# Kernel tuning notes

Measured on AMD Instinct MI355X. Metric: run time of the kernel, lower is better.

Reference implementation:

```python
import math
import jax, jax.numpy as jnp
import numpy as np

S, D = 4096, 2048
H, DH = 16, 128
ROPE_BASE = 10000.0


def _rotate_half(x):
    # x: [..., dh]; pairs (x1, x2) -> (-x2, x1), interleaved
    shp = x.shape
    x = x.reshape(*shp[:-1], shp[-1] // 2, 2)
    x1, x2 = x[..., 0], x[..., 1]
    return jnp.stack((-x2, x1), axis=-1).reshape(shp)


def _rope_cos_sin(seq_len, dh):
    inv_freq = 1.0 / (ROPE_BASE ** (jnp.arange(0, dh, 2, dtype=jnp.float32) / dh))
    t = jnp.arange(seq_len, dtype=jnp.float32)
    freqs = jnp.einsum('i,j->ij', t, inv_freq)  # [S, dh/2]
    cos = jnp.repeat(jnp.cos(freqs), 2, axis=-1)  # [S, dh]
    sin = jnp.repeat(jnp.sin(freqs), 2, axis=-1)
    return cos, sin


def setup_inputs() -> dict:
    key = jax.random.key(0)
    kx, kq, kk, kv, ko = jax.random.split(key, 5)
    scale_in = 1.0 / math.sqrt(D)
    scale_hd = 1.0 / math.sqrt(H * DH)
    return {
        'x': jax.random.normal(kx, (S, D), dtype=jnp.float32),
        'mask': jnp.tril(jnp.ones((S, S), dtype=bool)),  # causal
        'wq': jax.random.normal(kq, (H * DH, D), dtype=jnp.float32) * scale_in,
        'wk': jax.random.normal(kk, (H * DH, D), dtype=jnp.float32) * scale_in,
        'wv': jax.random.normal(kv, (H * DH, D), dtype=jnp.float32) * scale_in,
        'wo': jax.random.normal(ko, (D, H * DH), dtype=jnp.float32) * scale_hd,
    }


def reference(x, mask, wq, wk, wv, wo):
    s = x.shape[0]
    # QKV projections (Linear: y = W @ x per token) -> [h, S, dh]
    q = (x @ wq.T).reshape(s, H, DH).transpose(1, 0, 2)
    k = (x @ wk.T).reshape(s, H, DH).transpose(1, 0, 2)
    v = (x @ wv.T).reshape(s, H, DH).transpose(1, 0, 2)
    # RoPE
    cos, sin = _rope_cos_sin(s, DH)  # [S, dh] each
    q = q * cos[None] + _rotate_half(q) * sin[None]
    k = k * cos[None] + _rotate_half(k) * sin[None]
    # Attention
    sim = jnp.einsum('hid,hjd->hij', q, k) / math.sqrt(DH)  # [h, S, S]
    sim = jnp.where(mask[None], sim, -jnp.inf)
    attn = jax.nn.softmax(sim, axis=-1)
    out = jnp.einsum('hij,hjd->ihd', attn, v).reshape(s, H * DH)
    return out @ wo.T
```

## Files before the change

### kernel.cpp

```cpp
#include <hip/hip_runtime.h>
#include <stdint.h>

#define S_LEN 4096
#define D_MODEL 2048
#define NH 16
#define DH 128

typedef short s16x8 __attribute__((ext_vector_type(8)));
typedef short s16x2 __attribute__((ext_vector_type(2)));
typedef unsigned short u16;
typedef unsigned short u16x4 __attribute__((ext_vector_type(4)));
typedef float f32x4 __attribute__((ext_vector_type(4)));

__device__ __forceinline__ u16 f2bf(float f) {
  union { float f; uint32_t u; } v; v.f = f;
  uint32_t u = v.u;
  u += 0x7FFFu + ((u >> 16) & 1u);
  return (u16)(u >> 16);
}

__device__ __forceinline__ float bf2f(u16 b) {
  union { uint32_t u; float f; } v; v.u = ((uint32_t)b) << 16;
  return v.f;
}

__device__ __forceinline__ void async_copy16(const u16* g, u16* l) {
  __builtin_amdgcn_global_load_lds(
      (const __attribute__((address_space(1))) unsigned int*)g,
      (__attribute__((address_space(3))) unsigned int*)l, 16, 0, 0);
}

__global__ void cast_kernel(const float4* __restrict__ src, u16* __restrict__ dst, int n4) {
  int i = blockIdx.x * blockDim.x + threadIdx.x;
  if (i >= n4) return;
  float4 v = src[i];
  u16x4 o;
  o[0] = f2bf(v.x); o[1] = f2bf(v.y); o[2] = f2bf(v.z); o[3] = f2bf(v.w);
  *(u16x4*)(dst + (size_t)i * 4) = o;
}

__global__ void cast4_kernel(const float4* __restrict__ s0, const float4* __restrict__ s1,
                             const float4* __restrict__ s2, const float4* __restrict__ s3,
                             u16* __restrict__ d0, u16* __restrict__ d1,
                             u16* __restrict__ d2, u16* __restrict__ d3) {
  int b = blockIdx.x;
  int which = b >> 12;
  const float4* src = which == 0 ? s0 : which == 1 ? s1 : which == 2 ? s2 : s3;
  u16* dst = which == 0 ? d0 : which == 1 ? d1 : which == 2 ? d2 : d3;
  int i = (b & 4095) * blockDim.x + threadIdx.x;
  float4 v = src[i];
  u16x4 o;
  o[0] = f2bf(v.x); o[1] = f2bf(v.y); o[2] = f2bf(v.z); o[3] = f2bf(v.w);
  *(u16x4*)(dst + (size_t)i * 4) = o;
}

__global__ void rope_table(float* __restrict__ ctab, float* __restrict__ stab) {
  int idx = blockIdx.x * blockDim.x + threadIdx.x;
  int t = idx >> 6, p = idx & 63;
  float invf = powf(10000.0f, -(float)p / 64.0f);
  float th = (float)t * invf;
  ctab[idx] = cosf(th);
  stab[idx] = sinf(th);
}

#define PH_LGK0() do { asm volatile("s_waitcnt lgkmcnt(0)" ::: "memory"); \
                       __builtin_amdgcn_sched_barrier(0); } while (0)

__device__ __forceinline__ void stage16k(const u16* __restrict__ src, u16* dstbase,
                                         const int K) {
  const int tid = threadIdx.x;
  int rr = tid >> 3;
  int gc = ((tid & 7) ^ (rr & 7)) << 3;
  const u16* s = src + (size_t)rr * K + gc;
  u16* d = dstbase + (tid << 3);
  async_copy16(s, d);
  async_copy16(s + (size_t)64 * K, d + 4096);
}

__device__ __forceinline__ void mma256x128(
    const u16* __restrict__ Ab, const u16* __restrict__ Bb,
    const int K, u16* lds, f32x4 (&acc)[4][4])
{
  const int tid = threadIdx.x;
  const int lane = tid & 63, quad = lane >> 4, l16 = lane & 15;
  const int w = tid >> 6, wr = w >> 1, wc = w & 1;

  u16* const A0 = lds;
  u16* const B0 = lds + 16384;
  u16* const A1 = lds + 24576;
  u16* const B1 = lds + 40960;
  const int NT = K >> 6;

  auto sA = [&](int t, u16* buf) {
    int tc = t < NT ? t : NT - 1;
    stage16k(Ab + ((size_t)tc << 6), buf, K);
    stage16k(Ab + (size_t)128 * K + ((size_t)tc << 6), buf + 8192, K);
  };
  auto sB = [&](int t, u16* buf) {
    int tc = t < NT ? t : NT - 1;
    stage16k(Bb + ((size_t)tc << 6), buf, K);
  };

  s16x8 aC[4][2], aN[4][2], bA[2][2], bB0[2][2], bB1[2][2];

  auto rdA = [&](const u16* buf, s16x8 (&a)[4][2]) {
#pragma unroll
    for (int mt = 0; mt < 4; ++mt) {
      int ra = (wr << 6) + (mt << 4) + l16;
#pragma unroll
      for (int ks = 0; ks < 2; ++ks)
        a[mt][ks] = *(const s16x8*)(buf + (ra << 6) + ((((ks << 2) + quad) ^ (ra & 7)) << 3));
    }
  };
  auto rdBh = [&](const u16* buf, int nh, s16x8 (&b)[2][2]) {
#pragma unroll
    for (int nt = 0; nt < 2; ++nt) {
      int rb = (wc << 6) + (((nh << 1) + nt) << 4) + l16;
#pragma unroll
      for (int ks = 0; ks < 2; ++ks)
        b[nt][ks] = *(const s16x8*)(buf + (rb << 6) + ((((ks << 2) + quad) ^ (rb & 7)) << 3));
    }
  };
  auto mmah = [&](s16x8 (&a)[4][2], s16x8 (&b)[2][2], int nh) {
#pragma unroll
    for (int mt = 0; mt < 4; ++mt)
#pragma unroll
      for (int nt = 0; nt < 2; ++nt)
#pragma unroll
        for (int ks = 0; ks < 2; ++ks)
          acc[mt][(nh << 1) + nt] = __builtin_amdgcn_mfma_f32_16x16x32_bf16(
              a[mt][ks], b[nt][ks], acc[mt][(nh << 1) + nt], 0, 0, 0);
  };

  sA(0, A0); sB(0, B0); sA(1, A1); sB(1, B1);
  asm volatile("s_waitcnt vmcnt(6)" ::: "memory");
  __builtin_amdgcn_s_barrier();
  rdA(A0, aC); rdBh(B0, 0, bA); rdBh(B0, 1, bB0);

  const int NI = K >> 7;
#pragma unroll 1
  for (int i = 0; i < NI; ++i) {
    const int t0 = 2 * i, t1 = 2 * i + 1;
    __builtin_amdgcn_s_barrier();
    PH_LGK0();
    __builtin_amdgcn_s_setprio(1);
    mmah(aC, bA, 0);
    __builtin_amdgcn_s_setprio(0);
    asm volatile("s_waitcnt vmcnt(0)" ::: "memory");
    __builtin_amdgcn_s_barrier();
    __builtin_amdgcn_s_barrier();
    PH_LGK0();
    __builtin_amdgcn_s_setprio(1);
    sA(t0 + 2, A0); sB(t0 + 2, B0);
    rdA(A1, aN); rdBh(B1, 0, bA); rdBh(B1, 1, bB1);
    mmah(aC, bB0, 1);
    __builtin_amdgcn_s_setprio(0);
    __builtin_amdgcn_s_barrier();
    __builtin_amdgcn_s_barrier();
    PH_LGK0();
    __builtin_amdgcn_s_setprio(1);
    mmah(aN, bA, 0);
    __builtin_amdgcn_s_setprio(0);
    asm volatile("s_waitcnt vmcnt(0)" ::: "memory");
    __builtin_amdgcn_s_barrier();
    __builtin_amdgcn_s_barrier();
    PH_LGK0();
    __builtin_amdgcn_s_setprio(1);
    sA(t1 + 2, A1); sB(t1 + 2, B1);
    if (i + 1 < NI) { rdA(A0, aC); rdBh(B0, 0, bA); rdBh(B0, 1, bB0); }
    mmah(aN, bB1, 1);
    __builtin_amdgcn_s_setprio(0);
    __builtin_amdgcn_s_barrier();
  }
}

__global__ __launch_bounds__(512) void gemm256_qkv(
    const u16* __restrict__ A,
    const u16* __restrict__ wqb, const u16* __restrict__ wkb, const u16* __restrict__ wvb,
    u16* __restrict__ qh, u16* __restrict__ kh, u16* __restrict__ vh,
    const float* __restrict__ ctab, const float* __restrict__ stab)
{
  __shared__ __align__(16) u16 lds[49152];
  const int tid = threadIdx.x;
  const int lane = tid & 63, quad = lane >> 4, l16 = lane & 15;
  const int w = tid >> 6, wr = w >> 1, wc = w & 1;
  const int m0 = blockIdx.x << 8;
  const int by = blockIdx.y;
  const int which = by >> 4;
  const int n0 = (by & 15) << 7;
  const u16* B = which == 0 ? wqb : which == 1 ? wkb : wvb;
  u16* outp = which == 0 ? qh : which == 1 ? kh : vh;

  f32x4 acc[4][4];
  f32x4 zero = {0.f, 0.f, 0.f, 0.f};
#pragma unroll
  for (int i = 0; i < 4; ++i)
#pragma unroll
    for (int j = 0; j < 4; ++j) acc[i][j] = zero;

  mma256x128(A + (size_t)m0 * D_MODEL, B + (size_t)n0 * D_MODEL, D_MODEL, lds, acc);

#pragma unroll
  for (int mt = 0; mt < 4; ++mt) {
    int rowg = m0 + (wr << 6) + (mt << 4) + (quad << 2);
#pragma unroll
    for (int nt = 0; nt < 4; ++nt) {
      int cl = n0 + (wc << 6) + (nt << 4) + l16;
      int hh = cl >> 7, dd = cl & 127;
      int p = dd >> 1;
      f32x4 v = acc[mt][nt];
#pragma unroll
      for (int r = 0; r < 4; ++r) {
        float val = v[r];
        if (which < 2) {
          float partner = __shfl_xor(val, 1);
          float c = ctab[(size_t)(rowg + r) * 64 + p];
          float s = stab[(size_t)(rowg + r) * 64 + p];
          val = (dd & 1) ? fmaf(val, c, partner * s) : fmaf(val, c, -partner * s);
        }
        outp[((size_t)hh * S_LEN + (rowg + r)) * DH + dd] = f2bf(val);
      }
    }
  }
}

__global__ __launch_bounds__(512) void gemm256_out(
    const u16* __restrict__ A, const u16* __restrict__ B, float* __restrict__ outF)
{
  __shared__ __align__(16) u16 lds[49152];
  const int tid = threadIdx.x;
  const int lane = tid & 63, quad = lane >> 4, l16 = lane & 15;
  const int w = tid >> 6, wr = w >> 1, wc = w & 1;
  const int m0 = blockIdx.x << 8, n0 = blockIdx.y << 7;

  f32x4 acc[4][4];
  f32x4 zero = {0.f, 0.f, 0.f, 0.f};
#pragma unroll
  for (int i = 0; i < 4; ++i)
#pragma unroll
    for (int j = 0; j < 4; ++j) acc[i][j] = zero;

  mma256x128(A + (size_t)m0 * D_MODEL, B + (size_t)n0 * D_MODEL, D_MODEL, lds, acc);

#pragma unroll
  for (int mt = 0; mt < 4; ++mt) {
    int rowg = m0 + (wr << 6) + (mt << 4) + (quad << 2);
#pragma unroll
    for (int nt = 0; nt < 4; ++nt) {
      int col = n0 + (wc << 6) + (nt << 4) + l16;
      f32x4 v = acc[mt][nt];
#pragma unroll
      for (int r = 0; r < 4; ++r) outF[(size_t)(rowg + r) * D_MODEL + col] = v[r];
    }
  }
}

__global__ __launch_bounds__(512) void attn_kernel(
    const u16* __restrict__ Q, const u16* __restrict__ Kb,
    const u16* __restrict__ V,
    u16* __restrict__ U0, u16* __restrict__ U1, float* __restrict__ lbuf)
{
  __shared__ __align__(16) u16 lk[2][64 * 128];
  __shared__ __align__(16) u16 lvt[2][128 * 64];
  __shared__ __align__(16) u16 lp[8 * 1024];

  const int tid = threadIdx.x;
  const int w = tid >> 6, lane = tid & 63, quad = lane >> 4, l16 = lane & 15;
  const int h = blockIdx.y;
  const int bx = blockIdx.x;

  const u16* Qh = Q + (size_t)h * S_LEN * DH;
  const u16* Kh = Kb + (size_t)h * S_LEN * DH;
  const u16* Vh = V + (size_t)h * S_LEN * DH;

  const float scale = 0.08838834764831845f;
  const s16x8 vones = {0x3F80, 0x3F80, 0x3F80, 0x3F80, 0x3F80, 0x3F80, 0x3F80, 0x3F80};
  f32x4 zero = {0.f, 0.f, 0.f, 0.f};
  u16* lpw = lp + (w << 10);

  for (int seg = 0; seg < 2; ++seg) {
    const int qt = seg ? bx : (31 - bx);
    const int jlo = seg ? (qt + 1) : 0;
    const int jhi = seg ? (2 * qt + 2) : (qt + 1);
    const int i0 = qt << 7;
    const int iw = i0 + (w << 4);

    s16x8 qf[4];
#pragma unroll
    for (int ks = 0; ks < 4; ++ks)
      qf[ks] = *(const s16x8*)(Qh + (size_t)(iw + l16) * DH + ks * 32 + quad * 8);

    f32x4 accO[8];
#pragma unroll
    for (int dt = 0; dt < 8; ++dt) accO[dt] = zero;
    f32x4 accL = zero;

    {
      const int j0 = jlo << 6;
      int u = tid & 31, c8 = tid >> 5, r0 = u << 1;
      s16x8 v0 = *(const s16x8*)(Vh + (size_t)(j0 + r0) * DH + (c8 << 3));
      s16x8 v1 = *(const s16x8*)(Vh + (size_t)(j0 + r0 + 1) * DH + (c8 << 3));
#pragma unroll
      for (int rnd = 0; rnd < 2; ++rnd) {
        int c = rnd * 512 + tid;
        int r = c >> 4, cc = c & 15;
        int gcol = ((cc ^ (r & 15)) << 3);
        async_copy16(Kh + (size_t)(j0 + r) * DH + gcol, lk[0] + ((rnd * 512 + w * 64) << 3));
      }
      int cc = r0 >> 3;
#pragma unroll
      for (int e = 0; e < 8; ++e) {
        int d = (c8 << 3) + e;
        int off = (d << 6) + ((cc ^ (d & 7)) << 3) + (r0 & 7);
        s16x2 pr = {v0[e], v1[e]};
        *(s16x2*)(lvt[0] + off) = pr;
      }
    }
    __syncthreads();

    int cur = 0;
    for (int jt = jlo; jt < jhi; ++jt) {
      const int j0 = jt << 6;
      const bool has_next = (jt + 1) < jhi;

      s16x8 nv0, nv1;
      if (has_next) {
        const int nj0 = (jt + 1) << 6;
        int u = tid & 31, c8 = tid >> 5, r0 = u << 1;
        nv0 = *(const s16x8*)(Vh + (size_t)(nj0 + r0) * DH + (c8 << 3));
        nv1 = *(const s16x8*)(Vh + (size_t)(nj0 + r0 + 1) * DH + (c8 << 3));
#pragma unroll
        for (int rnd = 0; rnd < 2; ++rnd) {
          int c = rnd * 512 + tid;
          int r = c >> 4, cc = c & 15;
          int gcol = ((cc ^ (r & 15)) << 3);
          async_copy16(Kh + (size_t)(nj0 + r) * DH + gcol,
                       lk[cur ^ 1] + ((rnd * 512 + w * 64) << 3));
        }
      }

      const u16* lkc = lk[cur];
      f32x4 sa[4];
#pragma unroll
      for (int nt = 0; nt < 4; ++nt) sa[nt] = zero;
      __builtin_amdgcn_s_setprio(1);
#pragma unroll
      for (int ks = 0; ks < 4; ++ks) {
#pragma unroll
        for (int nt = 0; nt < 4; ++nt) {
          int row = (nt << 4) + l16;
          s16x8 kf = *(const s16x8*)(lkc + (row << 7) + ((((ks << 2) + quad) ^ (row & 15)) << 3));
          sa[nt] = __builtin_amdgcn_mfma_f32_16x16x32_bf16(qf[ks], kf, sa[nt], 0, 0, 0);
        }
      }
      __builtin_amdgcn_s_setprio(0);

      const bool maskt = (j0 + 63 > iw);
#pragma unroll
      for (int nt = 0; nt < 4; ++nt) {
        int col = (nt << 4) + l16;
        int j = j0 + col;
        int ccp = col >> 3;
#pragma unroll
        for (int r = 0; r < 4; ++r) {
          float raw = sa[nt][r];
          if (maskt) {
            int i = iw + (quad << 2) + r;
            if (j > i) raw = -1.0e30f;
          }
          float p = __expf(fmaf(raw, scale, -8.0f));
          union { float f; uint32_t u; } pv; pv.f = p;
          int m = (quad << 2) + r;
          lpw[(m << 6) + ((ccp ^ (m & 7)) << 3) + (col & 7)] = (u16)(pv.u >> 16);
        }
      }
      asm volatile("s_waitcnt lgkmcnt(0)" ::: "memory");
      s16x8 pf[2];
#pragma unroll
      for (int kp = 0; kp < 2; ++kp)
        pf[kp] = *(const s16x8*)(lpw + (l16 << 6) + ((((kp << 2) + quad) ^ (l16 & 7)) << 3));

      if (has_next) {
        int u = tid & 31, c8 = tid >> 5, r0 = u << 1;
        int cc = r0 >> 3;
        u16* dst = lvt[cur ^ 1];
#pragma unroll
        for (int e = 0; e < 8; ++e) {
          int d = (c8 << 3) + e;
          int off = (d << 6) + ((cc ^ (d & 7)) << 3) + (r0 & 7);
          s16x2 pr = {nv0[e], nv1[e]};
          *(s16x2*)(dst + off) = pr;
        }
      }

      const u16* lvc = lvt[cur];
      __builtin_amdgcn_s_setprio(1);
      accL = __builtin_amdgcn_mfma_f32_16x16x32_bf16(pf[0], vones, accL, 0, 0, 0);
      accL = __builtin_amdgcn_mfma_f32_16x16x32_bf16(pf[1], vones, accL, 0, 0, 0);
#pragma unroll
      for (int dt = 0; dt < 8; ++dt) {
#pragma unroll
        for (int kp = 0; kp < 2; ++kp) {
          int row = (dt << 4) + l16;
          s16x8 vf = *(const s16x8*)(lvc + (row << 6) + ((((kp << 2) + quad) ^ (row & 7)) << 3));
          accO[dt] = __builtin_amdgcn_mfma_f32_16x16x32_bf16(pf[kp], vf, accO[dt], 0, 0, 0);
        }
      }
      __builtin_amdgcn_s_setprio(0);

      __syncthreads();
      cur ^= 1;
    }

    u16* Useg = seg ? U1 : U0;
    float* ls = lbuf + (size_t)seg * NH * S_LEN + (size_t)h * S_LEN;
#pragma unroll
    for (int r = 0; r < 4; ++r) {
      float lr = accL[r];
      float inv = lr > 0.f ? 1.0f / lr : 0.f;
      int srow = iw + (quad << 2) + r;
#pragma unroll
      for (int dt = 0; dt < 8; ++dt)
        Useg[((size_t)h * S_LEN + srow) * DH + (dt << 4) + l16] = f2bf(accO[dt][r] * inv);
      if (l16 == 0) ls[srow] = lr;
    }
  }
}

__global__ void combine_kernel(const u16* __restrict__ U0, const u16* __restrict__ U1,
                               const float* __restrict__ lbuf, u16* __restrict__ ob)
{
  int t = blockIdx.x * 256 + threadIdx.x;
  int d8 = t & 15;
  int h = (t >> 4) & 15;
  int s = t >> 8;
  float l0 = lbuf[(size_t)h * S_LEN + s];
  float l1 = lbuf[(size_t)(NH * S_LEN) + (size_t)h * S_LEN + s];
  float inv = 1.0f / (l0 + l1);
  float w0 = l0 * inv, w1 = l1 * inv;
  size_t base = ((size_t)h * S_LEN + s) * DH + d8 * 8;
  s16x8 u0 = *(const s16x8*)(U0 + base);
  s16x8 u1 = *(const s16x8*)(U1 + base);
  u16 o[8];
#pragma unroll
  for (int e = 0; e < 8; ++e)
    o[e] = f2bf(w0 * bf2f((u16)u0[e]) + w1 * bf2f((u16)u1[e]));
  *(s16x8*)(ob + ((size_t)s * D_MODEL + h * DH + d8 * 8)) = *(s16x8*)o;
}

extern "C" void kernel_launch(void* const* d_in, const int* in_sizes, int n_in,
                              void* d_out, int out_size, void* d_ws, size_t ws_size,
                              hipStream_t stream) {
  const float* x  = (const float*)d_in[0];
  const float* wq = (const float*)d_in[2];
  const float* wk = (const float*)d_in[3];
  const float* wv = (const float*)d_in[4];
  const float* wo = (const float*)d_in[5];
  float* out = (float*)d_out;

  char* ws = (char*)d_ws;
  u16* xb  = (u16*)(ws);
  u16* wqb = (u16*)(ws + (16ull << 20));
  u16* wkb = (u16*)(ws + (24ull << 20));
  u16* wvb = (u16*)(ws + (32ull << 20));
  u16* wob = (u16*)(ws + (40ull << 20));
  u16* qh  = (u16*)(ws + (48ull << 20));
  u16* kh  = (u16*)(ws + (64ull << 20));
  u16* vh  = (u16*)(ws + (80ull << 20));
  float* ctab = (float*)(ws + (96ull << 20));
  float* stab = (float*)(ws + (97ull << 20));
  u16* U0 = (u16*)(ws);
  u16* U1 = (u16*)(ws + (16ull << 20));
  float* lbuf = (float*)(ws + (32ull << 20));
  u16* ob = qh;

  const int nx4 = S_LEN * D_MODEL / 4;
  cast_kernel<<<nx4 / 256, 256, 0, stream>>>((const float4*)x, xb, nx4);
  cast4_kernel<<<4 * 4096, 256, 0, stream>>>(
      (const float4*)wq, (const float4*)wk, (const float4*)wv, (const float4*)wo,
      wqb, wkb, wvb, wob);
  rope_table<<<(S_LEN * 64) / 256, 256, 0, stream>>>(ctab, stab);

  gemm256_qkv<<<dim3(S_LEN / 256, 3 * D_MODEL / 128), 512, 0, stream>>>(
      xb, wqb, wkb, wvb, qh, kh, vh, ctab, stab);

  attn_kernel<<<dim3(32, NH), 512, 0, stream>>>(qh, kh, vh, U0, U1, lbuf);
  combine_kernel<<<S_LEN * NH * 16 / 256, 256, 0, stream>>>(U0, U1, lbuf, ob);

  gemm256_out<<<dim3(S_LEN / 256, D_MODEL / 128), 512, 0, stream>>>(
      ob, wob, out);
}
```

Baseline: 481.4 us.

## Double attention query tile to 256 rows per block and remap heads to blocks

Each warp now handles 32 query rows (two 16-row sub-tiles) instead of 16, so each block covers 256 query rows and reuses every K/V tile loaded into shared memory across twice as many MFMAs. The grid drops from 512 to 256 blocks, launched as a 1D grid whose linear index is remapped to head and tile, presumably to spread heads across XCDs/L2. The intent is to halve K/V global and LDS traffic per unit of work. The cost is roughly doubled accumulator registers and P-buffer LDS, which may lower occupancy, and only 256 blocks to fill the GPU.

```diff
diff --git a/kernel.cpp b/kernel.cpp
--- a/kernel.cpp
+++ b/kernel.cpp
@@ -262,12 +262,14 @@
 {
   __shared__ __align__(16) u16 lk[2][64 * 128];
   __shared__ __align__(16) u16 lvt[2][128 * 64];
-  __shared__ __align__(16) u16 lp[8 * 1024];
+  __shared__ __align__(16) u16 lp[8 * 2048];
 
   const int tid = threadIdx.x;
   const int w = tid >> 6, lane = tid & 63, quad = lane >> 4, l16 = lane & 15;
-  const int h = blockIdx.y;
-  const int bx = blockIdx.x;
+  const int linear = blockIdx.x;
+  const int slot = linear >> 3;
+  const int h = ((linear & 7) << 1) | (slot >> 4);
+  const int bx = slot & 15;
 
   const u16* Qh = Q + (size_t)h * S_LEN * DH;
   const u16* Kh = Kb + (size_t)h * S_LEN * DH;
@@ -276,24 +278,28 @@
   const float scale = 0.08838834764831845f;
   const s16x8 vones = {0x3F80, 0x3F80, 0x3F80, 0x3F80, 0x3F80, 0x3F80, 0x3F80, 0x3F80};
   f32x4 zero = {0.f, 0.f, 0.f, 0.f};
-  u16* lpw = lp + (w << 10);
+  u16* lpw = lp + (w << 11);
 
   for (int seg = 0; seg < 2; ++seg) {
-    const int qt = seg ? bx : (31 - bx);
-    const int jlo = seg ? (qt + 1) : 0;
-    const int jhi = seg ? (2 * qt + 2) : (qt + 1);
-    const int i0 = qt << 7;
-    const int iw = i0 + (w << 4);
-
-    s16x8 qf[4];
-#pragma unroll
-    for (int ks = 0; ks < 4; ++ks)
-      qf[ks] = *(const s16x8*)(Qh + (size_t)(iw + l16) * DH + ks * 32 + quad * 8);
-
-    f32x4 accO[8];
-#pragma unroll
-    for (int dt = 0; dt < 8; ++dt) accO[dt] = zero;
-    f32x4 accL = zero;
+    const int qt = seg ? bx : (15 - bx);
+    const int jlo = seg ? (2 * qt + 2) : 0;
+    const int jhi = seg ? (4 * qt + 4) : (2 * qt + 2);
+    const int i0 = qt << 8;
+    const int iws = i0 + (w << 5);
+
+    s16x8 qf[2][4];
+#pragma unroll
+    for (int s = 0; s < 2; ++s)
+#pragma unroll
+      for (int ks = 0; ks < 4; ++ks)
+        qf[s][ks] = *(const s16x8*)(Qh + (size_t)(iws + (s << 4) + l16) * DH + ks * 32 + quad * 8);
+
+    f32x4 accO[2][8];
+#pragma unroll
+    for (int s = 0; s < 2; ++s)
+#pragma unroll
+      for (int dt = 0; dt < 8; ++dt) accO[s][dt] = zero;
+    f32x4 accL[2] = {zero, zero};
 
     {
       const int j0 = jlo << 6;
@@ -340,9 +346,11 @@
       }
 
       const u16* lkc = lk[cur];
-      f32x4 sa[4];
-#pragma unroll
-      for (int nt = 0; nt < 4; ++nt) sa[nt] = zero;
+      f32x4 sa[2][4];
+#pragma unroll
+      for (int s = 0; s < 2; ++s)
+#pragma unroll
+        for (int nt = 0; nt < 4; ++nt) sa[s][nt] = zero;
       __builtin_amdgcn_s_setprio(1);
 #pragma unroll
       for (int ks = 0; ks < 4; ++ks) {
@@ -350,35 +358,44 @@
         for (int nt = 0; nt < 4; ++nt) {
           int row = (nt << 4) + l16;
           s16x8 kf = *(const s16x8*)(lkc + (row << 7) + ((((ks << 2) + quad) ^ (row & 15)) << 3));
-          sa[nt] = __builtin_amdgcn_mfma_f32_16x16x32_bf16(qf[ks], kf, sa[nt], 0, 0, 0);
+          sa[0][nt] = __builtin_amdgcn_mfma_f32_16x16x32_bf16(qf[0][ks], kf, sa[0][nt], 0, 0, 0);
+          sa[1][nt] = __builtin_amdgcn_mfma_f32_16x16x32_bf16(qf[1][ks], kf, sa[1][nt], 0, 0, 0);
         }
       }
       __builtin_amdgcn_s_setprio(0);
 
-      const bool maskt = (j0 + 63 > iw);
-#pragma unroll
-      for (int nt = 0; nt < 4; ++nt) {
-        int col = (nt << 4) + l16;
-        int j = j0 + col;
-        int ccp = col >> 3;
-#pragma unroll
-        for (int r = 0; r < 4; ++r) {
-          float raw = sa[nt][r];
-          if (maskt) {
-            int i = iw + (quad << 2) + r;
-            if (j > i) raw = -1.0e30f;
+#pragma unroll
+      for (int s = 0; s < 2; ++s) {
+        const int iw = iws + (s << 4);
+        const bool maskt = (j0 + 63 > iw);
+        u16* lps = lpw + (s << 10);
+#pragma unroll
+        for (int nt = 0; nt < 4; ++nt) {
+          int col = (nt << 4) + l16;
+          int j = j0 + col;
+          int ccp = col >> 3;
+#pragma unroll
+          for (int r = 0; r < 4; ++r) {
+            float raw = sa[s][nt][r];
+            if (maskt) {
+              int i = iw + (quad << 2) + r;
+              if (j > i) raw = -1.0e30f;
+            }
+            float p = __expf(fmaf(raw, scale, -8.0f));
+            union { float f; uint32_t u; } pv; pv.f = p;
+            int m = (quad << 2) + r;
+            lps[(m << 6) + ((ccp ^ (m & 7)) << 3) + (col & 7)] = (u16)(pv.u >> 16);
           }
-          float p = __expf(fmaf(raw, scale, -8.0f));
-          union { float f; uint32_t u; } pv; pv.f = p;
-          int m = (quad << 2) + r;
-          lpw[(m << 6) + ((ccp ^ (m & 7)) << 3) + (col & 7)] = (u16)(pv.u >> 16);
         }
       }
       asm volatile("s_waitcnt lgkmcnt(0)" ::: "memory");
-      s16x8 pf[2];
-#pragma unroll
-      for (int kp = 0; kp < 2; ++kp)
-        pf[kp] = *(const s16x8*)(lpw + (l16 << 6) + ((((kp << 2) + quad) ^ (l16 & 7)) << 3));
+      s16x8 pf[2][2];
+#pragma unroll
+      for (int s = 0; s < 2; ++s)
+#pragma unroll
+        for (int kp = 0; kp < 2; ++kp)
+          pf[s][kp] = *(const s16x8*)(lpw + (s << 10) + (l16 << 6) +
+                                      ((((kp << 2) + quad) ^ (l16 & 7)) << 3));
 
       if (has_next) {
         int u = tid & 31, c8 = tid >> 5, r0 = u << 1;
@@ -395,15 +412,18 @@
 
       const u16* lvc = lvt[cur];
       __builtin_amdgcn_s_setprio(1);
-      accL = __builtin_amdgcn_mfma_f32_16x16x32_bf16(pf[0], vones, accL, 0, 0, 0);
-      accL = __builtin_amdgcn_mfma_f32_16x16x32_bf16(pf[1], vones, accL, 0, 0, 0);
+      accL[0] = __builtin_amdgcn_mfma_f32_16x16x32_bf16(pf[0][0], vones, accL[0], 0, 0, 0);
+      accL[0] = __builtin_amdgcn_mfma_f32_16x16x32_bf16(pf[0][1], vones, accL[0], 0, 0, 0);
+      accL[1] = __builtin_amdgcn_mfma_f32_16x16x32_bf16(pf[1][0], vones, accL[1], 0, 0, 0);
+      accL[1] = __builtin_amdgcn_mfma_f32_16x16x32_bf16(pf[1][1], vones, accL[1], 0, 0, 0);
 #pragma unroll
       for (int dt = 0; dt < 8; ++dt) {
 #pragma unroll
         for (int kp = 0; kp < 2; ++kp) {
           int row = (dt << 4) + l16;
           s16x8 vf = *(const s16x8*)(lvc + (row << 6) + ((((kp << 2) + quad) ^ (row & 7)) << 3));
-          accO[dt] = __builtin_amdgcn_mfma_f32_16x16x32_bf16(pf[kp], vf, accO[dt], 0, 0, 0);
+          accO[0][dt] = __builtin_amdgcn_mfma_f32_16x16x32_bf16(pf[0][kp], vf, accO[0][dt], 0, 0, 0);
+          accO[1][dt] = __builtin_amdgcn_mfma_f32_16x16x32_bf16(pf[1][kp], vf, accO[1][dt], 0, 0, 0);
         }
       }
       __builtin_amdgcn_s_setprio(0);
@@ -415,14 +435,18 @@
     u16* Useg = seg ? U1 : U0;
     float* ls = lbuf + (size_t)seg * NH * S_LEN + (size_t)h * S_LEN;
 #pragma unroll
-    for (int r = 0; r < 4; ++r) {
-      float lr = accL[r];
-      float inv = lr > 0.f ? 1.0f / lr : 0.f;
-      int srow = iw + (quad << 2) + r;
-#pragma unroll
-      for (int dt = 0; dt < 8; ++dt)
-        Useg[((size_t)h * S_LEN + srow) * DH + (dt << 4) + l16] = f2bf(accO[dt][r] * inv);
-      if (l16 == 0) ls[srow] = lr;
+    for (int s = 0; s < 2; ++s) {
+      const int iw = iws + (s << 4);
+#pragma unroll
+      for (int r = 0; r < 4; ++r) {
+        float lr = accL[s][r];
+        float inv = lr > 0.f ? 1.0f / lr : 0.f;
+        int srow = iw + (quad << 2) + r;
+#pragma unroll
+        for (int dt = 0; dt < 8; ++dt)
+          Useg[((size_t)h * S_LEN + srow) * DH + (dt << 4) + l16] = f2bf(accO[s][dt][r] * inv);
+        if (l16 == 0) ls[srow] = lr;
+      }
     }
   }
 }
@@ -484,7 +508,7 @@
   gemm256_qkv<<<dim3(S_LEN / 256, 3 * D_MODEL / 128), 512, 0, stream>>>(
       xb, wqb, wkb, wvb, qh, kh, vh, ctab, stab);
 
-  attn_kernel<<<dim3(32, NH), 512, 0, stream>>>(qh, kh, vh, U0, U1, lbuf);
+  attn_kernel<<<dim3(256), 512, 0, stream>>>(qh, kh, vh, U0, U1, lbuf);
   combine_kernel<<<S_LEN * NH * 16 / 256, 256, 0, stream>>>(U0, U1, lbuf, ob);
 
   gemm256_out<<<dim3(S_LEN / 256, D_MODEL / 128), 512, 0, stream>>>(
```

After: 430.3 us. -10.6%, faster.
